# Kernel optimization log

Hardware: AMD Instinct MI355X
Metric: run time of the kernel (lower is better)

## Reference

```python
import jax, jax.numpy as jnp
import numpy as np

N_NODES = 50000
DEG = 16
N_EDGES = N_NODES * DEG
H = 8
D = 32
NEG_SLOPE = 0.2


def setup_inputs() -> dict:
    key = jax.random.key(0)
    k1, k2, k3, k4 = jax.random.split(key, 4)
    feat = jax.random.normal(k1, (N_NODES, H * D), dtype=jnp.float32)
    attn_l = jax.random.normal(k2, (1, H, D), dtype=jnp.float32) * 0.1
    attn_r = jax.random.normal(k3, (1, H, D), dtype=jnp.float32) * 0.1
    bias = jnp.zeros((H * D,), dtype=jnp.float32)
    # every dst node has in-degree DEG (no zero-in-degree nodes)
    dst = jnp.repeat(jnp.arange(N_NODES, dtype=jnp.int32), DEG)
    src = jax.random.randint(k4, (N_EDGES,), 0, N_NODES, dtype=jnp.int32)
    return {"feat": feat, "attn_l": attn_l, "attn_r": attn_r, "bias": bias,
            "src": src, "dst": dst}


def reference(feat, attn_l, attn_r, bias, src, dst):
    N = feat.shape[0]
    fs = feat.reshape(N, H, D)                      # [N,H,D]
    el = (fs * attn_l).sum(-1)                      # [N,H]
    er = (fs * attn_r).sum(-1)                      # [N,H]
    # per-edge attention logit: u_add_v + leaky_relu
    e = jax.nn.leaky_relu(el[src] + er[dst], negative_slope=NEG_SLOPE)  # [E,H]
    # segmented (per-dst) softmax over incoming edges
    emax = jax.ops.segment_max(e, dst, num_segments=N)  # [N,H]
    ee = jnp.exp(e - emax[dst])                         # [E,H]
    esum = jax.ops.segment_sum(ee, dst, num_segments=N)  # [N,H]
    a = ee / esum[dst]                                  # [E,H]
    # u_mul_e then sum: weighted scatter-aggregate
    msg = fs[src] * a[:, :, None]                       # [E,H,D]
    rst = jax.ops.segment_sum(msg, dst, num_segments=N)  # [N,H,D]
    rst = rst + bias.reshape(1, H, D)
    return rst
```

## Files before the change

kernel.cpp:

```cpp
#include <hip/hip_runtime.h>

#define HEADS 8
#define DIM 32
#define DEGREE 16
#define NEG_SLOPE 0.2f

__device__ __forceinline__ unsigned short f2bf(float f) {
  unsigned u = __float_as_uint(f);
  unsigned r = (u + 0x7fffu + ((u >> 16) & 1u)) >> 16;
  return (unsigned short)r;
}
__device__ __forceinline__ float bf2f(unsigned short b) {
  return __uint_as_float(((unsigned)b) << 16);
}

template <bool WRITE_BF16>
__global__ __launch_bounds__(256) void elr_kernel(
    const float4* __restrict__ feat4,
    const float4* __restrict__ attn_l4,
    const float4* __restrict__ attn_r4,
    float* __restrict__ elT, float* __restrict__ erT,
    ushort4* __restrict__ featb, int total4, int N) {
  int t = blockIdx.x * 256 + threadIdx.x;
  if (t >= total4) return;
  float4 v = feat4[t];
  int c4 = t & 63;
  float4 al = attn_l4[c4];
  float4 ar = attn_r4[c4];
  float pl = v.x * al.x + v.y * al.y + v.z * al.z + v.w * al.w;
  float pr = v.x * ar.x + v.y * ar.y + v.z * ar.z + v.w * ar.w;
#pragma unroll
  for (int off = 4; off >= 1; off >>= 1) {
    pl += __shfl_xor(pl, off);
    pr += __shfl_xor(pr, off);
  }
  if ((t & 7) == 0) {
    int n = t >> 6;
    int h = c4 >> 3;
    elT[h * N + n] = pl;
    erT[h * N + n] = pr;
  }
  if (WRITE_BF16) {
    ushort4 b;
    b.x = f2bf(v.x); b.y = f2bf(v.y); b.z = f2bf(v.z); b.w = f2bf(v.w);
    featb[t] = b;
  }
}

__global__ __launch_bounds__(256) void gat_sliced_kernel(
    const uint4* __restrict__ featb,
    const float* __restrict__ elT,
    const float* __restrict__ erT,
    const int* __restrict__ srcIdx,
    const float* __restrict__ bias,
    float* __restrict__ out, int N) {
  int lane = threadIdx.x & 63;
  int wave = threadIdx.x >> 6;
  int h = blockIdx.x & 7;
  int chunk = blockIdx.x >> 3;
  int g = lane >> 4;
  int l16 = lane & 15;
  int n = chunk * 16 + wave * 4 + g;
  bool ok = (n < N);

  int sidx = 0;
  float w = 0.0f;
  if (ok) {
    sidx = srcIdx[n * DEGREE + l16];
    float e = elT[h * N + sidx] + erT[h * N + n];
    e = e > 0.0f ? e : NEG_SLOPE * e;
    float m = e;
#pragma unroll
    for (int off = 8; off >= 1; off >>= 1) m = fmaxf(m, __shfl_xor(m, off));
    float x = __expf(e - m);
    float s = x;
#pragma unroll
    for (int off = 8; off >= 1; off >>= 1) s += __shfl_xor(s, off);
    w = x / s;
  }

  if (ok) {
    int q = (lane >> 2) & 3;
    int c = lane & 3;
    int base = lane & 48;
    float acc[8];
#pragma unroll
    for (int k = 0; k < 8; k++) acc[k] = 0.0f;
#pragma unroll
    for (int p = 0; p < 4; p++) {
      int j = p * 4 + q;
      int sj = __shfl(sidx, base + j);
      float wj = __shfl(w, base + j);
      uint4 r = featb[(size_t)sj * 32 + h * 4 + c];
      acc[0] += wj * __uint_as_float(r.x << 16);
      acc[1] += wj * __uint_as_float(r.x & 0xffff0000u);
      acc[2] += wj * __uint_as_float(r.y << 16);
      acc[3] += wj * __uint_as_float(r.y & 0xffff0000u);
      acc[4] += wj * __uint_as_float(r.z << 16);
      acc[5] += wj * __uint_as_float(r.z & 0xffff0000u);
      acc[6] += wj * __uint_as_float(r.w << 16);
      acc[7] += wj * __uint_as_float(r.w & 0xffff0000u);
    }
#pragma unroll
    for (int k = 0; k < 8; k++) {
      acc[k] += __shfl_xor(acc[k], 4);
      acc[k] += __shfl_xor(acc[k], 8);
    }
    if (q == 0) {
      const float4* bias4 = (const float4*)bias;
      int bidx = h * 8 + c * 2;
      float4 b0 = bias4[bidx], b1 = bias4[bidx + 1];
      float4 o0 = make_float4(acc[0] + b0.x, acc[1] + b0.y,
                              acc[2] + b0.z, acc[3] + b0.w);
      float4 o1 = make_float4(acc[4] + b1.x, acc[5] + b1.y,
                              acc[6] + b1.z, acc[7] + b1.w);
      size_t o = (size_t)n * 64 + h * 8 + c * 2;
      ((float4*)out)[o] = o0;
      ((float4*)out)[o + 1] = o1;
    }
  }
}

__global__ __launch_bounds__(256) void gat_f32_kernel(
    const float4* __restrict__ featv,
    const float* __restrict__ elT,
    const float* __restrict__ erT,
    const int* __restrict__ srcIdx,
    const float* __restrict__ bias,
    float* __restrict__ out, int N) {
  int wave = threadIdx.x >> 6;
  int lane = threadIdx.x & 63;
  int n = blockIdx.x * 4 + wave;
  __shared__ float s_a[4][DEGREE][HEADS + 1];
  bool active = (n < N);
  int sidx = 0;
  if (active) {
    const int* s = srcIdx + n * DEGREE;
    int i = lane & 15;
    int hh = lane >> 4;
    sidx = s[i];
    float e0 = elT[hh * N + sidx]       + erT[hh * N + n];
    float e1 = elT[(hh + 4) * N + sidx] + erT[(hh + 4) * N + n];
    e0 = e0 > 0.0f ? e0 : NEG_SLOPE * e0;
    e1 = e1 > 0.0f ? e1 : NEG_SLOPE * e1;
    float m0 = e0, m1 = e1;
#pragma unroll
    for (int off = 8; off >= 1; off >>= 1) {
      m0 = fmaxf(m0, __shfl_xor(m0, off));
      m1 = fmaxf(m1, __shfl_xor(m1, off));
    }
    float x0 = __expf(e0 - m0), x1 = __expf(e1 - m1);
    float s0 = x0, s1 = x1;
#pragma unroll
    for (int off = 8; off >= 1; off >>= 1) {
      s0 += __shfl_xor(s0, off);
      s1 += __shfl_xor(s1, off);
    }
    s_a[wave][i][hh]     = x0 / s0;
    s_a[wave][i][hh + 4] = x1 / s1;
  }
  __syncthreads();
  if (active) {
    int h = lane >> 3;
    float4 acc = ((const float4*)bias)[lane];
#pragma unroll
    for (int j = 0; j < DEGREE; j++) {
      int sj = __shfl(sidx, j);
      float a = s_a[wave][j][h];
      float4 v = featv[(size_t)sj * 64 + lane];
      acc.x += a * v.x; acc.y += a * v.y; acc.z += a * v.z; acc.w += a * v.w;
    }
    ((float4*)out)[(size_t)n * 64 + lane] = acc;
  }
}

extern "C" void kernel_launch(void* const* d_in, const int* in_sizes, int n_in,
                              void* d_out, int out_size, void* d_ws, size_t ws_size,
                              hipStream_t stream) {
  const float* feat   = (const float*)d_in[0];
  const float* attn_l = (const float*)d_in[1];
  const float* attn_r = (const float*)d_in[2];
  const float* bias   = (const float*)d_in[3];
  const int*   src    = (const int*)d_in[4];
  float* out = (float*)d_out;

  int total = in_sizes[0];
  int N = total / (HEADS * DIM);
  int total4 = total / 4;

  float* elT = (float*)d_ws;
  float* erT = elT + (size_t)N * HEADS;
  ushort4* featb = (ushort4*)(erT + (size_t)N * HEADS);

  size_t need = (size_t)N * HEADS * 2 * sizeof(float) + (size_t)total * 2;
  bool use_bf16 = (ws_size >= need);

  if (use_bf16) {
    elr_kernel<true><<<(total4 + 255) / 256, 256, 0, stream>>>(
        (const float4*)feat, (const float4*)attn_l, (const float4*)attn_r,
        elT, erT, featb, total4, N);
    int nchunks = (N + 15) / 16;
    gat_sliced_kernel<<<nchunks * 8, 256, 0, stream>>>(
        (const uint4*)featb, elT, erT, src, bias, out, N);
  } else {
    elr_kernel<false><<<(total4 + 255) / 256, 256, 0, stream>>>(
        (const float4*)feat, (const float4*)attn_l, (const float4*)attn_r,
        elT, erT, nullptr, total4, N);
    int nb = (N + 3) / 4;
    gat_f32_kernel<<<nb, 256, 0, stream>>>(
        (const float4*)feat, elT, erT, src, bias, out, N);
  }
}
```

Baseline: 193.8 us.

## Store bf16 features head-major and stage source indices in LDS

```diff
diff --git a/kernel.cpp b/kernel.cpp
--- a/kernel.cpp
+++ b/kernel.cpp
@@ -9,9 +9,6 @@
   unsigned u = __float_as_uint(f);
   unsigned r = (u + 0x7fffu + ((u >> 16) & 1u)) >> 16;
   return (unsigned short)r;
-}
-__device__ __forceinline__ float bf2f(unsigned short b) {
-  return __uint_as_float(((unsigned)b) << 16);
 }
 
 template <bool WRITE_BF16>
@@ -20,7 +17,7 @@
     const float4* __restrict__ attn_l4,
     const float4* __restrict__ attn_r4,
     float* __restrict__ elT, float* __restrict__ erT,
-    ushort4* __restrict__ featb, int total4, int N) {
+    ushort4* __restrict__ featbH, int total4, int N) {
   int t = blockIdx.x * 256 + threadIdx.x;
   if (t >= total4) return;
   float4 v = feat4[t];
@@ -34,90 +31,95 @@
     pl += __shfl_xor(pl, off);
     pr += __shfl_xor(pr, off);
   }
+  int n = t >> 6;
+  int h = c4 >> 3;
   if ((t & 7) == 0) {
-    int n = t >> 6;
-    int h = c4 >> 3;
     elT[h * N + n] = pl;
     erT[h * N + n] = pr;
   }
   if (WRITE_BF16) {
     ushort4 b;
     b.x = f2bf(v.x); b.y = f2bf(v.y); b.z = f2bf(v.z); b.w = f2bf(v.w);
-    featb[t] = b;
-  }
-}
-
-__global__ __launch_bounds__(256) void gat_sliced_kernel(
-    const uint4* __restrict__ featb,
+    int d4 = c4 & 7;
+    featbH[((size_t)h * N + n) * 8 + d4] = b;
+  }
+}
+
+__global__ __launch_bounds__(256) void gat_hmajor_kernel(
+    const uint4* __restrict__ featbH,
     const float* __restrict__ elT,
     const float* __restrict__ erT,
     const int* __restrict__ srcIdx,
     const float* __restrict__ bias,
     float* __restrict__ out, int N) {
-  int lane = threadIdx.x & 63;
-  int wave = threadIdx.x >> 6;
   int h = blockIdx.x & 7;
   int chunk = blockIdx.x >> 3;
+  int tid = threadIdx.x;
+  __shared__ int s_src[16][DEGREE];
+  {
+    int nl = tid >> 4, e = tid & 15;
+    int nn = chunk * 16 + nl;
+    s_src[nl][e] = (nn < N) ? srcIdx[nn * DEGREE + e] : 0;
+  }
+  __syncthreads();
+
+  int lane = tid & 63;
+  int wave = tid >> 6;
   int g = lane >> 4;
   int l16 = lane & 15;
-  int n = chunk * 16 + wave * 4 + g;
-  bool ok = (n < N);
-
-  int sidx = 0;
-  float w = 0.0f;
-  if (ok) {
-    sidx = srcIdx[n * DEGREE + l16];
-    float e = elT[h * N + sidx] + erT[h * N + n];
-    e = e > 0.0f ? e : NEG_SLOPE * e;
-    float m = e;
-#pragma unroll
-    for (int off = 8; off >= 1; off >>= 1) m = fmaxf(m, __shfl_xor(m, off));
-    float x = __expf(e - m);
-    float s = x;
-#pragma unroll
-    for (int off = 8; off >= 1; off >>= 1) s += __shfl_xor(s, off);
-    w = x / s;
-  }
-
-  if (ok) {
-    int q = (lane >> 2) & 3;
-    int c = lane & 3;
-    int base = lane & 48;
-    float acc[8];
-#pragma unroll
-    for (int k = 0; k < 8; k++) acc[k] = 0.0f;
-#pragma unroll
-    for (int p = 0; p < 4; p++) {
-      int j = p * 4 + q;
-      int sj = __shfl(sidx, base + j);
-      float wj = __shfl(w, base + j);
-      uint4 r = featb[(size_t)sj * 32 + h * 4 + c];
-      acc[0] += wj * __uint_as_float(r.x << 16);
-      acc[1] += wj * __uint_as_float(r.x & 0xffff0000u);
-      acc[2] += wj * __uint_as_float(r.y << 16);
-      acc[3] += wj * __uint_as_float(r.y & 0xffff0000u);
-      acc[4] += wj * __uint_as_float(r.z << 16);
-      acc[5] += wj * __uint_as_float(r.z & 0xffff0000u);
-      acc[6] += wj * __uint_as_float(r.w << 16);
-      acc[7] += wj * __uint_as_float(r.w & 0xffff0000u);
-    }
-#pragma unroll
-    for (int k = 0; k < 8; k++) {
-      acc[k] += __shfl_xor(acc[k], 4);
-      acc[k] += __shfl_xor(acc[k], 8);
-    }
-    if (q == 0) {
-      const float4* bias4 = (const float4*)bias;
-      int bidx = h * 8 + c * 2;
-      float4 b0 = bias4[bidx], b1 = bias4[bidx + 1];
-      float4 o0 = make_float4(acc[0] + b0.x, acc[1] + b0.y,
-                              acc[2] + b0.z, acc[3] + b0.w);
-      float4 o1 = make_float4(acc[4] + b1.x, acc[5] + b1.y,
-                              acc[6] + b1.z, acc[7] + b1.w);
-      size_t o = (size_t)n * 64 + h * 8 + c * 2;
-      ((float4*)out)[o] = o0;
-      ((float4*)out)[o + 1] = o1;
-    }
+  int nl = wave * 4 + g;
+  int n = chunk * 16 + nl;
+  if (n >= N) return;
+
+  int sidx = s_src[nl][l16];
+  float e = elT[h * N + sidx] + erT[h * N + n];
+  e = e > 0.0f ? e : NEG_SLOPE * e;
+  float m = e;
+#pragma unroll
+  for (int off = 8; off >= 1; off >>= 1) m = fmaxf(m, __shfl_xor(m, off));
+  float x = __expf(e - m);
+  float s = x;
+#pragma unroll
+  for (int off = 8; off >= 1; off >>= 1) s += __shfl_xor(s, off);
+  float w = x / s;
+
+  int q = (lane >> 2) & 3;
+  int c = lane & 3;
+  int base = lane & 48;
+  float acc[8];
+#pragma unroll
+  for (int k = 0; k < 8; k++) acc[k] = 0.0f;
+#pragma unroll
+  for (int p = 0; p < 4; p++) {
+    int j = p * 4 + q;
+    int sj = __shfl(sidx, base + j);
+    float wj = __shfl(w, base + j);
+    uint4 r = featbH[((size_t)h * N + sj) * 4 + c];
+    acc[0] += wj * __uint_as_float(r.x << 16);
+    acc[1] += wj * __uint_as_float(r.x & 0xffff0000u);
+    acc[2] += wj * __uint_as_float(r.y << 16);
+    acc[3] += wj * __uint_as_float(r.y & 0xffff0000u);
+    acc[4] += wj * __uint_as_float(r.z << 16);
+    acc[5] += wj * __uint_as_float(r.z & 0xffff0000u);
+    acc[6] += wj * __uint_as_float(r.w << 16);
+    acc[7] += wj * __uint_as_float(r.w & 0xffff0000u);
+  }
+#pragma unroll
+  for (int k = 0; k < 8; k++) {
+    acc[k] += __shfl_xor(acc[k], 4);
+    acc[k] += __shfl_xor(acc[k], 8);
+  }
+  if (q == 0) {
+    const float4* bias4 = (const float4*)bias;
+    int bidx = h * 8 + c * 2;
+    float4 b0 = bias4[bidx], b1 = bias4[bidx + 1];
+    float4 o0 = make_float4(acc[0] + b0.x, acc[1] + b0.y,
+                            acc[2] + b0.z, acc[3] + b0.w);
+    float4 o1 = make_float4(acc[4] + b1.x, acc[5] + b1.y,
+                            acc[6] + b1.z, acc[7] + b1.w);
+    size_t o = (size_t)n * 64 + h * 8 + c * 2;
+    ((float4*)out)[o] = o0;
+    ((float4*)out)[o + 1] = o1;
   }
 }
 
@@ -190,7 +192,7 @@
 
   float* elT = (float*)d_ws;
   float* erT = elT + (size_t)N * HEADS;
-  ushort4* featb = (ushort4*)(erT + (size_t)N * HEADS);
+  ushort4* featbH = (ushort4*)(erT + (size_t)N * HEADS);
 
   size_t need = (size_t)N * HEADS * 2 * sizeof(float) + (size_t)total * 2;
   bool use_bf16 = (ws_size >= need);
@@ -198,10 +200,10 @@
   if (use_bf16) {
     elr_kernel<true><<<(total4 + 255) / 256, 256, 0, stream>>>(
         (const float4*)feat, (const float4*)attn_l, (const float4*)attn_r,
-        elT, erT, featb, total4, N);
+        elT, erT, featbH, total4, N);
     int nchunks = (N + 15) / 16;
-    gat_sliced_kernel<<<nchunks * 8, 256, 0, stream>>>(
-        (const uint4*)featb, elT, erT, src, bias, out, N);
+    gat_hmajor_kernel<<<nchunks * 8, 256, 0, stream>>>(
+        (const uint4*)featbH, elT, erT, src, bias, out, N);
   } else {
     elr_kernel<false><<<(total4 + 255) / 256, 256, 0, stream>>>(
         (const float4*)feat, (const float4*)attn_l, (const float4*)attn_r,
```

New measurement: 175.8 us. 9.3% less time.
